# Performance work log

Hardware: AMD Instinct MI355X
Metric: run time of the kernel (lower is better)

## Reference

```python
import jax, jax.numpy as jnp
import numpy as np

HID = 512


def _lstm_params(key, in_dim, hid):
    k = 1.0 / np.sqrt(hid)
    ks = jax.random.split(key, 4)
    W_ih = jax.random.uniform(ks[0], (4 * hid, in_dim), minval=-k, maxval=k)
    W_hh = jax.random.uniform(ks[1], (4 * hid, hid), minval=-k, maxval=k)
    b_ih = jax.random.uniform(ks[2], (4 * hid,), minval=-k, maxval=k)
    b_hh = jax.random.uniform(ks[3], (4 * hid,), minval=-k, maxval=k)
    return W_ih, W_hh, b_ih, b_hh


def _linear_params(key, in_dim, out_dim):
    k = 1.0 / np.sqrt(in_dim)
    k1, k2 = jax.random.split(key)
    W = jax.random.uniform(k1, (out_dim, in_dim), minval=-k, maxval=k)
    b = jax.random.uniform(k2, (out_dim,), minval=-k, maxval=k)
    return W, b


def setup_inputs() -> dict:
    key = jax.random.key(0)
    ks = jax.random.split(key, 8)
    state_action = jax.random.normal(ks[0], (32768, 19), dtype=jnp.float32)
    W_ih1, W_hh1, b_ih1, b_hh1 = _lstm_params(ks[1], 19, HID)
    W_ih2, W_hh2, b_ih2, b_hh2 = _lstm_params(ks[2], 19, HID)
    W_xyz, b_xyz = _linear_params(ks[3], HID, 3)
    W_zeta, b_zeta = _linear_params(ks[4], HID, 3)
    W_uvw, b_uvw = _linear_params(ks[5], HID, 3)
    W_pqr, b_pqr = _linear_params(ks[6], HID, 3)
    return dict(state_action=state_action,
                W_ih1=W_ih1, W_hh1=W_hh1, b_ih1=b_ih1, b_hh1=b_hh1,
                W_ih2=W_ih2, W_hh2=W_hh2, b_ih2=b_ih2, b_hh2=b_hh2,
                W_xyz=W_xyz, b_xyz=b_xyz, W_zeta=W_zeta, b_zeta=b_zeta,
                W_uvw=W_uvw, b_uvw=b_uvw, W_pqr=W_pqr, b_pqr=b_pqr)


def _lstm_step(gates_x, h, c, W_hh, b_hh, hid):
    # torch LSTMCell gate order: input, forget, cell(g), output
    g = gates_x + h @ W_hh.T + b_hh
    i = jax.nn.sigmoid(g[:hid])
    f = jax.nn.sigmoid(g[hid:2 * hid])
    gg = jnp.tanh(g[2 * hid:3 * hid])
    o = jax.nn.sigmoid(g[3 * hid:])
    c_new = f * c + i * gg
    h_new = o * jnp.tanh(c_new)
    return h_new, c_new


def reference(state_action, W_ih1, W_hh1, b_ih1, b_hh1,
              W_ih2, W_hh2, b_ih2, b_hh2,
              W_xyz, b_xyz, W_zeta, b_zeta, W_uvw, b_uvw, W_pqr, b_pqr):
    hid = W_hh1.shape[1]
    # precompute input projections for all timesteps (one big GEMM each)
    gx1 = state_action @ W_ih1.T + b_ih1  # [H, 4*hid]
    gx2 = state_action @ W_ih2.T + b_ih2  # [H, 4*hid]

    def step(carry, gx):
        h1, c1, h2, c2 = carry
        g1, g2 = gx
        h1, c1 = _lstm_step(g1, h1, c1, W_hh1, b_hh1, hid)
        h2, c2 = _lstm_step(g2, h2, c2, W_hh2, b_hh2, hid)
        return (h1, c1, h2, c2), (h1, h2)

    z = jnp.zeros((hid,), dtype=state_action.dtype)
    _, (h1s, h2s) = jax.lax.scan(step, (z, z, z, z), (gx1, gx2))
    xyz = h1s @ W_xyz.T + b_xyz
    zeta = h2s @ W_zeta.T + b_zeta
    uvw = h1s @ W_uvw.T + b_uvw
    pqr = h2s @ W_pqr.T + b_pqr
    # original returns a list of [1,12] tensors; we return the stacked [H,12]
    return jnp.concatenate([xyz, zeta, uvw, pqr], axis=1)
```

## Files before the change

### kernel.cpp

```cpp
#include <hip/hip_runtime.h>

#define T_STEPS 32768
#define THREADS 256
#define NLAUNCH 256
#define D_SLOTS 4

typedef unsigned int uint32;
typedef unsigned long long ull;
typedef unsigned int u32x4 __attribute__((ext_vector_type(4)));


__device__ inline float fsig(float x) {
    return __builtin_amdgcn_rcpf(1.f + __expf(-x));
}
__device__ inline float ftanh(float x) {
    return 1.f - 2.f * __builtin_amdgcn_rcpf(1.f + __expf(2.f * x));
}
__device__ inline float wred64(float x) {
    x += __shfl_xor(x, 1);  x += __shfl_xor(x, 2);  x += __shfl_xor(x, 4);
    x += __shfl_xor(x, 8);  x += __shfl_xor(x, 16); x += __shfl_xor(x, 32);
    return x;
}

__device__ inline void poll4x(const ull* p, u32x4& v0, u32x4& v1, u32x4& v2, u32x4& v3) {
    asm volatile("global_load_dwordx4 %0, %4, off sc0 nt\n\t"
                 "global_load_dwordx4 %1, %4, off offset:1024 sc0 nt\n\t"
                 "global_load_dwordx4 %2, %4, off offset:2048 sc0 nt\n\t"
                 "global_load_dwordx4 %3, %4, off offset:3072 sc0 nt\n\t"
                 "s_waitcnt vmcnt(0)"
                 : "=&v"(v0), "=&v"(v1), "=&v"(v2), "=&v"(v3)
                 : "v"(p) : "memory");
}

__device__ inline uint32 a_add(uint32* p, uint32 v) {
    return __hip_atomic_fetch_add(p, v, __ATOMIC_RELAXED, __HIP_MEMORY_SCOPE_AGENT);
}
__device__ inline uint32 a_ld(const uint32* p) {
    return __hip_atomic_load(p, __ATOMIC_RELAXED, __HIP_MEMORY_SCOPE_AGENT);
}
__device__ inline void a_st(uint32* p, uint32 v) {
    __hip_atomic_store(p, v, __ATOMIC_RELAXED, __HIP_MEMORY_SCOPE_AGENT);
}
__device__ inline ull rescue_rmw(ull* p) {
    return __hip_atomic_fetch_add(p, 0ull, __ATOMIC_RELAXED, __HIP_MEMORY_SCOPE_AGENT);
}

__global__ __launch_bounds__(THREADS, 1)
void lstm_persistent(const float* __restrict__ sa,
                     const float* __restrict__ W_ih1, const float* __restrict__ W_hh1,
                     const float* __restrict__ b_ih1, const float* __restrict__ b_hh1,
                     const float* __restrict__ W_ih2, const float* __restrict__ W_hh2,
                     const float* __restrict__ b_ih2, const float* __restrict__ b_hh2,
                     const float* __restrict__ W_xyz, const float* __restrict__ b_xyz,
                     const float* __restrict__ W_zeta, const float* __restrict__ b_zeta,
                     const float* __restrict__ W_uvw, const float* __restrict__ b_uvw,
                     const float* __restrict__ W_pqr, const float* __restrict__ b_pqr,
                     float* __restrict__ out, ull* hrot, uint32* claim)
{
    const int tid  = threadIdx.x;
    const int wv   = tid >> 6;
    const int lane = tid & 63;

    __shared__ int s_lstm, s_w;

    if (tid == 0) {
        uint32 xcc;
        asm volatile("s_getreg_b32 %0, hwreg(HW_REG_XCC_ID)" : "=s"(xcc));
        xcc &= 7;
        uint32* cnt     = claim;
        uint32* rankcnt = claim + 8;
        uint32* grank   = claim + 16;

        int lstm = -1, w = 0;
        uint32 slot = a_add(&cnt[xcc], 1);
        if (slot < 32) {
            w = (int)slot;
            if (slot == 31) {
                uint32 rank = a_add(rankcnt, 1);
                a_st(&grank[xcc], (rank < 2) ? (rank + 1) : 0xFEu);
            }
            uint32 g;
            long spins = 0;
            for (;;) {
                g = a_ld(&grank[xcc]);
                if (g != 0) break;
                if (a_ld(rankcnt) >= 2 && ++spins > 200000) { g = 0xFEu; break; }
            }
            if (g != 0xFEu) lstm = (int)g - 1;
        }
        s_lstm = lstm; s_w = w;
    }
    __syncthreads();
    const int lstm = s_lstm;
    const int w    = s_w;
    if (lstm < 0) return;

    const float* W_ih = lstm ? W_ih2 : W_ih1;
    const float* W_hh = lstm ? W_hh2 : W_hh1;
    const float* b_ih = lstm ? b_ih2 : b_ih1;
    const float* b_hh = lstm ? b_hh2 : b_hh1;
    const float* W_a  = lstm ? W_zeta : W_xyz;
    const float* W_b  = lstm ? W_pqr  : W_uvw;

    ull* hb = hrot + (size_t)lstm * D_SLOTS * 512;

    __shared__ __align__(16) float hw_all[4][528];
    __shared__ float wih_lds[64 * 19];
    __shared__ float pj_lds[6 * 512];
    float* hw = hw_all[wv];

    const int r  = lane >> 2;
    const int cb = lane & 3;
    const int gt = r >> 2;
    const int jj = r & 3;
    const int G  = gt * 512 + (w << 4) + (wv << 2) + jj;

    float wa[128];
    {
        const float4* wp4 = (const float4*)(W_hh + (size_t)G * 512 + cb * 128);
        #pragma unroll
        for (int k = 0; k < 32; ++k) {
            float4 t4 = wp4[k];
            asm volatile("v_accvgpr_write_b32 %0, %1" : "=a"(wa[4 * k + 0]) : "v"(t4.x));
            asm volatile("v_accvgpr_write_b32 %0, %1" : "=a"(wa[4 * k + 1]) : "v"(t4.y));
            asm volatile("v_accvgpr_write_b32 %0, %1" : "=a"(wa[4 * k + 2]) : "v"(t4.z));
            asm volatile("v_accvgpr_write_b32 %0, %1" : "=a"(wa[4 * k + 3]) : "v"(t4.w));
        }
    }
    for (int idx = tid; idx < 64 * 19; idx += THREADS) {
        int rr = idx / 19, kk = idx - rr * 19;
        int v2 = rr >> 4, r2 = rr & 15;
        int G2 = (r2 >> 2) * 512 + (w << 4) + (v2 << 2) + (r2 & 3);
        wih_lds[idx] = W_ih[G2 * 19 + kk];
    }
    for (int idx = tid; idx < 6 * 512; idx += THREADS) {
        int o = idx >> 9, c = idx & 511;
        pj_lds[idx] = (o < 3) ? W_a[o * 512 + c] : W_b[(o - 3) * 512 + c];
    }
    const float bsum = b_ih[G] + b_hh[G];

    float ball[16];
    #pragma unroll
    for (int k = 0; k < 16; ++k)
        asm volatile("v_accvgpr_write_b32 %0, %1" : "=a"(ball[k]) : "v"(bsum));

    float pb[6] = {0.f, 0.f, 0.f, 0.f, 0.f, 0.f};
    if (wv == 1) {
        const float* ba = lstm ? b_zeta : b_xyz;
        const float* bb = lstm ? b_pqr  : b_uvw;
        #pragma unroll
        for (int o = 0; o < 3; ++o) { pb[o] = ba[o]; pb[o + 3] = bb[o]; }
    }

    float c_reg = 0.0f;
    int   thr   = 64;
    __syncthreads();

    const bool projector = (wv == 1);

    for (int t = 0; t <= T_STEPS; ++t) {
        if (t == T_STEPS && !(projector && w == ((T_STEPS - 1) & 31))) break;

        float sav = 0.f;
        if (lane < 19 && t < T_STEPS) sav = sa[(size_t)t * 19 + lane];

        if (t > 0) {
            ull* sp = hb + (size_t)((uint32)(t - 1) & (D_SLOTS - 1)) * 512 + 2 * lane;
            const uint32 tag = (uint32)t;
            u32x4 v0, v1, v2, v3;
            int spin = 0;
            for (;;) {
                poll4x(sp, v0, v1, v2, v3);
                if (v0.x == tag && v0.z == tag && v1.x == tag && v1.z == tag &&
                    v2.x == tag && v2.z == tag && v3.x == tag && v3.z == tag) break;
                if (++spin >= thr) {
                    ull a0 = rescue_rmw(sp),       a1 = rescue_rmw(sp + 1);
                    ull b0 = rescue_rmw(sp + 128), b1 = rescue_rmw(sp + 129);
                    ull c0 = rescue_rmw(sp + 256), c1 = rescue_rmw(sp + 257);
                    ull d0 = rescue_rmw(sp + 384), d1 = rescue_rmw(sp + 385);
                    if ((uint32)a0 == tag && (uint32)a1 == tag &&
                        (uint32)b0 == tag && (uint32)b1 == tag &&
                        (uint32)c0 == tag && (uint32)c1 == tag &&
                        (uint32)d0 == tag && (uint32)d1 == tag) {
                        v0.y = (uint32)(a0 >> 32); v0.w = (uint32)(a1 >> 32);
                        v1.y = (uint32)(b0 >> 32); v1.w = (uint32)(b1 >> 32);
                        v2.y = (uint32)(c0 >> 32); v2.w = (uint32)(c1 >> 32);
                        v3.y = (uint32)(d0 >> 32); v3.w = (uint32)(d1 >> 32);
                        break;
                    }
                    thr = 2;
                    spin = 0;
                }
            }
            *(float2*)&hw[      2 * lane] = make_float2(__uint_as_float(v0.y), __uint_as_float(v0.w));
            *(float2*)&hw[132 + 2 * lane] = make_float2(__uint_as_float(v1.y), __uint_as_float(v1.w));
            *(float2*)&hw[264 + 2 * lane] = make_float2(__uint_as_float(v2.y), __uint_as_float(v2.w));
            *(float2*)&hw[396 + 2 * lane] = make_float2(__uint_as_float(v3.y), __uint_as_float(v3.w));
        } else if (t == 0) {
            *(float2*)&hw[      2 * lane] = make_float2(0.f, 0.f);
            *(float2*)&hw[132 + 2 * lane] = make_float2(0.f, 0.f);
            *(float2*)&hw[264 + 2 * lane] = make_float2(0.f, 0.f);
            *(float2*)&hw[396 + 2 * lane] = make_float2(0.f, 0.f);
        }

        if (t < T_STEPS) {
            float part = (cb == 0) ? bsum : 0.f;
            {
                const int base = (wv * 16 + r) * 19;
                const int k0 = cb * 5;
                #pragma unroll
                for (int i = 0; i < 5; ++i) {
                    int k = k0 + i;
                    if (k < 19) part = fmaf(__shfl(sav, k), wih_lds[base + k], part);
                }
            }
            {
                const float4* hp4 = (const float4*)&hw[cb * 132];
                float ax = 0.f, ay = 0.f, az = 0.f, aw2 = 0.f;
                #pragma unroll
                for (int k = 0; k < 32; ++k) {
                    float4 hv = hp4[k];
                    float w0, w1, w2, w3;
                    asm volatile("v_accvgpr_read_b32 %0, %1" : "=v"(w0) : "a"(wa[4 * k + 0]));
                    asm volatile("v_accvgpr_read_b32 %0, %1" : "=v"(w1) : "a"(wa[4 * k + 1]));
                    asm volatile("v_accvgpr_read_b32 %0, %1" : "=v"(w2) : "a"(wa[4 * k + 2]));
                    asm volatile("v_accvgpr_read_b32 %0, %1" : "=v"(w3) : "a"(wa[4 * k + 3]));
                    ax  = fmaf(w0, hv.x, ax);
                    ay  = fmaf(w1, hv.y, ay);
                    az  = fmaf(w2, hv.z, az);
                    aw2 = fmaf(w3, hv.w, aw2);
                }
                part += (ax + ay) + (az + aw2);
            }
            part += __shfl_xor(part, 1);
            part += __shfl_xor(part, 2);

            float act = (gt == 2) ? ftanh(part) : fsig(part);
            float i_v = __shfl(act, 4 * jj);
            float f_v = __shfl(act, 16 + 4 * jj);
            float g_v = __shfl(act, 32 + 4 * jj);
            float o_v = __shfl(act, 48 + 4 * jj);

            if (r < 4 && cb == 0) {
                c_reg = f_v * c_reg + i_v * g_v;
                float hn = o_v * ftanh(c_reg);
                ull pk = ((ull)__float_as_uint(hn) << 32) | (ull)(uint32)(t + 1);
                __hip_atomic_store(
                    &hb[(size_t)((uint32)t & (D_SLOTS - 1)) * 512 + (w << 4) + (wv << 2) + r],
                    pk, __ATOMIC_RELAXED, __HIP_MEMORY_SCOPE_WORKGROUP);
            }
        }

        if (t > 0 && projector && (((t - 1) & 31) == w)) {
            float a0 = 0.f, a1 = 0.f, a2 = 0.f, a3 = 0.f, a4 = 0.f, a5 = 0.f;
            #pragma unroll
            for (int m = 0; m < 8; ++m) {
                int c = lane + (m << 6);
                float hv = hw[((c >> 7) * 132) + (c & 127)];
                a0 = fmaf(hv, pj_lds[c],        a0);
                a1 = fmaf(hv, pj_lds[512 + c],  a1);
                a2 = fmaf(hv, pj_lds[1024 + c], a2);
                a3 = fmaf(hv, pj_lds[1536 + c], a3);
                a4 = fmaf(hv, pj_lds[2048 + c], a4);
                a5 = fmaf(hv, pj_lds[2560 + c], a5);
            }
            a0 = wred64(a0); a1 = wred64(a1); a2 = wred64(a2);
            a3 = wred64(a3); a4 = wred64(a4); a5 = wred64(a5);
            if (lane == 0) {
                size_t ob = (size_t)(t - 1) * 12;
                int ca = 3 * lstm, cbb = 6 + 3 * lstm;
                out[ob + ca + 0]  = a0 + pb[0];
                out[ob + ca + 1]  = a1 + pb[1];
                out[ob + ca + 2]  = a2 + pb[2];
                out[ob + cbb + 0] = a3 + pb[3];
                out[ob + cbb + 1] = a4 + pb[4];
                out[ob + cbb + 2] = a5 + pb[5];
            }
        }
    }

    if (lstm < -1) {
        float s = 0.f;
        #pragma unroll
        for (int k = 0; k < 16; ++k) {
            float tv;
            asm volatile("v_accvgpr_read_b32 %0, %1" : "=v"(tv) : "a"(ball[k]));
            s += tv;
        }
        ((float*)claim)[31] = s;
    }
}

extern "C" void kernel_launch(void* const* d_in, const int* in_sizes, int n_in,
                              void* d_out, int out_size, void* d_ws, size_t ws_size,
                              hipStream_t stream)
{
    const float* sa    = (const float*)d_in[0];
    const float* W_ih1 = (const float*)d_in[1];
    const float* W_hh1 = (const float*)d_in[2];
    const float* b_ih1 = (const float*)d_in[3];
    const float* b_hh1 = (const float*)d_in[4];
    const float* W_ih2 = (const float*)d_in[5];
    const float* W_hh2 = (const float*)d_in[6];
    const float* b_ih2 = (const float*)d_in[7];
    const float* b_hh2 = (const float*)d_in[8];
    const float* W_xyz = (const float*)d_in[9];
    const float* b_xyz = (const float*)d_in[10];
    const float* W_zeta= (const float*)d_in[11];
    const float* b_zeta= (const float*)d_in[12];
    const float* W_uvw = (const float*)d_in[13];
    const float* b_uvw = (const float*)d_in[14];
    const float* W_pqr = (const float*)d_in[15];
    const float* b_pqr = (const float*)d_in[16];

    float*  out   = (float*)d_out;
    ull*    hrot  = (ull*)d_ws;
    uint32* claim = (uint32*)((char*)d_ws + 2 * D_SLOTS * 512 * sizeof(ull));

    hipMemsetAsync(d_ws, 0, 2 * D_SLOTS * 512 * sizeof(ull) + 128, stream);

    lstm_persistent<<<NLAUNCH, THREADS, 0, stream>>>(
        sa, W_ih1, W_hh1, b_ih1, b_hh1, W_ih2, W_hh2, b_ih2, b_hh2,
        W_xyz, b_xyz, W_zeta, b_zeta, W_uvw, b_uvw, W_pqr, b_pqr,
        out, hrot, claim);
}
```

Before: 70.48 ms.

## Add per-wave ready flags, prefetch inputs, and split projection across waves

Producers now write their h values with one wave-wide vectorized store and then set a per-wave ready flag. Consumers poll a small flag array before reading the tagged h buffer, and the RMW rescue path is removed. The input-projection dot product is computed before the wait and the next timestep's input is prefetched, taking that work off the critical path. The output projection is spread across three waves and the slot ring is widened to 8. The extra flag round trip adds latency on every step, and dropping the rescue path risks stalls if stale cache lines persist.

```diff
diff --git a/kernel.cpp b/kernel.cpp
--- a/kernel.cpp
+++ b/kernel.cpp
@@ -3,11 +3,12 @@
 #define T_STEPS 32768
 #define THREADS 256
 #define NLAUNCH 256
-#define D_SLOTS 4
+#define D_SLOTS 8
 
 typedef unsigned int uint32;
 typedef unsigned long long ull;
 typedef unsigned int u32x4 __attribute__((ext_vector_type(4)));
+typedef unsigned int u32x2 __attribute__((ext_vector_type(2)));
 
 
 __device__ inline float fsig(float x) {
@@ -22,6 +23,11 @@
     return x;
 }
 
+__device__ inline void pollflag(const uint32* p, u32x2& f) {
+    asm volatile("global_load_dwordx2 %0, %1, off sc0 nt\n\t"
+                 "s_waitcnt vmcnt(0)"
+                 : "=v"(f) : "v"(p) : "memory");
+}
 __device__ inline void poll4x(const ull* p, u32x4& v0, u32x4& v1, u32x4& v2, u32x4& v3) {
     asm volatile("global_load_dwordx4 %0, %4, off sc0 nt\n\t"
                  "global_load_dwordx4 %1, %4, off offset:1024 sc0 nt\n\t"
@@ -40,9 +46,6 @@
 }
 __device__ inline void a_st(uint32* p, uint32 v) {
     __hip_atomic_store(p, v, __ATOMIC_RELAXED, __HIP_MEMORY_SCOPE_AGENT);
-}
-__device__ inline ull rescue_rmw(ull* p) {
-    return __hip_atomic_fetch_add(p, 0ull, __ATOMIC_RELAXED, __HIP_MEMORY_SCOPE_AGENT);
 }
 
 __global__ __launch_bounds__(THREADS, 1)
@@ -55,7 +58,7 @@
                      const float* __restrict__ W_zeta, const float* __restrict__ b_zeta,
                      const float* __restrict__ W_uvw, const float* __restrict__ b_uvw,
                      const float* __restrict__ W_pqr, const float* __restrict__ b_pqr,
-                     float* __restrict__ out, ull* hrot, uint32* claim)
+                     float* __restrict__ out, ull* hrot, uint32* ready, uint32* claim)
 {
     const int tid  = threadIdx.x;
     const int wv   = tid >> 6;
@@ -102,7 +105,8 @@
     const float* W_a  = lstm ? W_zeta : W_xyz;
     const float* W_b  = lstm ? W_pqr  : W_uvw;
 
-    ull* hb = hrot + (size_t)lstm * D_SLOTS * 512;
+    ull*    hb  = hrot  + (size_t)lstm * D_SLOTS * 512;
+    uint32* rdy = ready + lstm * (D_SLOTS * 128);
 
     __shared__ __align__(16) float hw_all[4][528];
     __shared__ float wih_lds[64 * 19];
@@ -144,53 +148,51 @@
     for (int k = 0; k < 16; ++k)
         asm volatile("v_accvgpr_write_b32 %0, %1" : "=a"(ball[k]) : "v"(bsum));
 
-    float pb[6] = {0.f, 0.f, 0.f, 0.f, 0.f, 0.f};
-    if (wv == 1) {
+    const int d0 = 2 * (wv - 1);
+    float pb0 = 0.f, pb1 = 0.f;
+    int   col0 = 0, col1 = 0;
+    if (wv >= 1) {
         const float* ba = lstm ? b_zeta : b_xyz;
         const float* bb = lstm ? b_pqr  : b_uvw;
-        #pragma unroll
-        for (int o = 0; o < 3; ++o) { pb[o] = ba[o]; pb[o + 3] = bb[o]; }
+        pb0  = (d0 < 3)     ? ba[d0]     : bb[d0 - 3];
+        pb1  = (d0 + 1 < 3) ? ba[d0 + 1] : bb[d0 - 2];
+        col0 = (d0 < 3)     ? 3 * lstm + d0       : 6 + 3 * lstm + (d0 - 3);
+        col1 = (d0 + 1 < 3) ? 3 * lstm + (d0 + 1) : 6 + 3 * lstm + (d0 - 2);
     }
 
     float c_reg = 0.0f;
-    int   thr   = 64;
     __syncthreads();
 
-    const bool projector = (wv == 1);
+    float sav = (lane < 19) ? sa[lane] : 0.f;
 
     for (int t = 0; t <= T_STEPS; ++t) {
-        if (t == T_STEPS && !(projector && w == ((T_STEPS - 1) & 31))) break;
-
-        float sav = 0.f;
-        if (lane < 19 && t < T_STEPS) sav = sa[(size_t)t * 19 + lane];
+        if (t == T_STEPS && !(wv >= 1 && ((t - 1) & 31) == w)) break;
+
+        float gxv = bsum;
+        if (t < T_STEPS) {
+            const int base = (wv * 16 + r) * 19;
+            #pragma unroll
+            for (int k = 0; k < 19; ++k)
+                gxv = fmaf(__shfl(sav, k), wih_lds[base + k], gxv);
+        }
+        float sav_n = 0.f;
+        if (lane < 19 && t + 1 < T_STEPS) sav_n = sa[(size_t)(t + 1) * 19 + lane];
 
         if (t > 0) {
-            ull* sp = hb + (size_t)((uint32)(t - 1) & (D_SLOTS - 1)) * 512 + 2 * lane;
-            const uint32 tag = (uint32)t;
+            const uint32 tag  = (uint32)t;
+            const int    slot = (int)((uint32)(t - 1) & (D_SLOTS - 1));
+            const uint32* fp  = rdy + slot * 128 + 2 * lane;
+            u32x2 f;
+            for (;;) {
+                pollflag(fp, f);
+                if (__all((f.x == tag) && (f.y == tag))) break;
+            }
+            ull* sp = hb + (size_t)slot * 512 + 2 * lane;
             u32x4 v0, v1, v2, v3;
-            int spin = 0;
             for (;;) {
                 poll4x(sp, v0, v1, v2, v3);
                 if (v0.x == tag && v0.z == tag && v1.x == tag && v1.z == tag &&
                     v2.x == tag && v2.z == tag && v3.x == tag && v3.z == tag) break;
-                if (++spin >= thr) {
-                    ull a0 = rescue_rmw(sp),       a1 = rescue_rmw(sp + 1);
-                    ull b0 = rescue_rmw(sp + 128), b1 = rescue_rmw(sp + 129);
-                    ull c0 = rescue_rmw(sp + 256), c1 = rescue_rmw(sp + 257);
-                    ull d0 = rescue_rmw(sp + 384), d1 = rescue_rmw(sp + 385);
-                    if ((uint32)a0 == tag && (uint32)a1 == tag &&
-                        (uint32)b0 == tag && (uint32)b1 == tag &&
-                        (uint32)c0 == tag && (uint32)c1 == tag &&
-                        (uint32)d0 == tag && (uint32)d1 == tag) {
-                        v0.y = (uint32)(a0 >> 32); v0.w = (uint32)(a1 >> 32);
-                        v1.y = (uint32)(b0 >> 32); v1.w = (uint32)(b1 >> 32);
-                        v2.y = (uint32)(c0 >> 32); v2.w = (uint32)(c1 >> 32);
-                        v3.y = (uint32)(d0 >> 32); v3.w = (uint32)(d1 >> 32);
-                        break;
-                    }
-                    thr = 2;
-                    spin = 0;
-                }
             }
             *(float2*)&hw[      2 * lane] = make_float2(__uint_as_float(v0.y), __uint_as_float(v0.w));
             *(float2*)&hw[132 + 2 * lane] = make_float2(__uint_as_float(v1.y), __uint_as_float(v1.w));
@@ -204,16 +206,7 @@
         }
 
         if (t < T_STEPS) {
-            float part = (cb == 0) ? bsum : 0.f;
-            {
-                const int base = (wv * 16 + r) * 19;
-                const int k0 = cb * 5;
-                #pragma unroll
-                for (int i = 0; i < 5; ++i) {
-                    int k = k0 + i;
-                    if (k < 19) part = fmaf(__shfl(sav, k), wih_lds[base + k], part);
-                }
-            }
+            float part = (cb == 0) ? gxv : 0.f;
             {
                 const float4* hp4 = (const float4*)&hw[cb * 132];
                 float ax = 0.f, ay = 0.f, az = 0.f, aw2 = 0.f;
@@ -241,42 +234,50 @@
             float g_v = __shfl(act, 32 + 4 * jj);
             float o_v = __shfl(act, 48 + 4 * jj);
 
+            float hn = 0.f;
             if (r < 4 && cb == 0) {
                 c_reg = f_v * c_reg + i_v * g_v;
-                float hn = o_v * ftanh(c_reg);
-                ull pk = ((ull)__float_as_uint(hn) << 32) | (ull)(uint32)(t + 1);
-                __hip_atomic_store(
-                    &hb[(size_t)((uint32)t & (D_SLOTS - 1)) * 512 + (w << 4) + (wv << 2) + r],
-                    pk, __ATOMIC_RELAXED, __HIP_MEMORY_SCOPE_WORKGROUP);
-            }
-        }
-
-        if (t > 0 && projector && (((t - 1) & 31) == w)) {
-            float a0 = 0.f, a1 = 0.f, a2 = 0.f, a3 = 0.f, a4 = 0.f, a5 = 0.f;
+                hn    = o_v * ftanh(c_reg);
+            }
+            {
+                const uint32 tag2 = (uint32)(t + 1);
+                float h1 = __shfl(hn, 4), h2 = __shfl(hn, 8), h3 = __shfl(hn, 12);
+                const int slot_t = (int)((uint32)t & (D_SLOTS - 1));
+                if (lane == 0) {
+                    ull* p = hb + (size_t)slot_t * 512 + (w << 4) + (wv << 2);
+                    u32x4 A, B;
+                    A.x = tag2; A.y = __float_as_uint(hn);
+                    A.z = tag2; A.w = __float_as_uint(h1);
+                    B.x = tag2; B.y = __float_as_uint(h2);
+                    B.z = tag2; B.w = __float_as_uint(h3);
+                    asm volatile("global_store_dwordx4 %0, %1, off sc0 nt\n\t"
+                                 "global_store_dwordx4 %2, %3, off sc0 nt"
+                                 :: "v"(p), "v"(A), "v"(p + 2), "v"(B) : "memory");
+                    asm volatile("s_waitcnt vmcnt(0)" ::: "memory");
+                    uint32* fq = rdy + slot_t * 128 + (w << 2) + wv;
+                    asm volatile("global_store_dword %0, %1, off sc0 nt"
+                                 :: "v"(fq), "v"(tag2) : "memory");
+                }
+            }
+        }
+
+        if (t > 0 && wv >= 1 && ((t - 1) & 31) == w) {
+            float a0 = 0.f, a1 = 0.f;
             #pragma unroll
             for (int m = 0; m < 8; ++m) {
                 int c = lane + (m << 6);
                 float hv = hw[((c >> 7) * 132) + (c & 127)];
-                a0 = fmaf(hv, pj_lds[c],        a0);
-                a1 = fmaf(hv, pj_lds[512 + c],  a1);
-                a2 = fmaf(hv, pj_lds[1024 + c], a2);
-                a3 = fmaf(hv, pj_lds[1536 + c], a3);
-                a4 = fmaf(hv, pj_lds[2048 + c], a4);
-                a5 = fmaf(hv, pj_lds[2560 + c], a5);
-            }
-            a0 = wred64(a0); a1 = wred64(a1); a2 = wred64(a2);
-            a3 = wred64(a3); a4 = wred64(a4); a5 = wred64(a5);
+                a0 = fmaf(hv, pj_lds[d0 * 512 + c],       a0);
+                a1 = fmaf(hv, pj_lds[(d0 + 1) * 512 + c], a1);
+            }
+            a0 = wred64(a0); a1 = wred64(a1);
             if (lane == 0) {
                 size_t ob = (size_t)(t - 1) * 12;
-                int ca = 3 * lstm, cbb = 6 + 3 * lstm;
-                out[ob + ca + 0]  = a0 + pb[0];
-                out[ob + ca + 1]  = a1 + pb[1];
-                out[ob + ca + 2]  = a2 + pb[2];
-                out[ob + cbb + 0] = a3 + pb[3];
-                out[ob + cbb + 1] = a4 + pb[4];
-                out[ob + cbb + 2] = a5 + pb[5];
-            }
-        }
+                out[ob + col0] = a0 + pb0;
+                out[ob + col1] = a1 + pb1;
+            }
+        }
+        sav = sav_n;
     }
 
     if (lstm < -1) {
@@ -315,12 +316,13 @@
 
     float*  out   = (float*)d_out;
     ull*    hrot  = (ull*)d_ws;
-    uint32* claim = (uint32*)((char*)d_ws + 2 * D_SLOTS * 512 * sizeof(ull));
-
-    hipMemsetAsync(d_ws, 0, 2 * D_SLOTS * 512 * sizeof(ull) + 128, stream);
+    uint32* ready = (uint32*)((char*)d_ws + 65536);
+    uint32* claim = (uint32*)((char*)d_ws + 65536 + 8192);
+
+    hipMemsetAsync(d_ws, 0, 65536 + 8192 + 128, stream);
 
     lstm_persistent<<<NLAUNCH, THREADS, 0, stream>>>(
         sa, W_ih1, W_hh1, b_ih1, b_hh1, W_ih2, W_hh2, b_ih2, b_hh2,
         W_xyz, b_xyz, W_zeta, b_zeta, W_uvw, b_uvw, W_pqr, b_pqr,
-        out, hrot, claim);
-}
+        out, hrot, ready, claim);
+}
```

Measured after the change: 77.82 ms. 10.4% more time.
